# Kernel optimization log

Hardware: AMD Instinct MI355X
Metric: run time of the kernel (lower is better)

The kernel has to match this reference:

```python
import jax, jax.numpy as jnp
import numpy as np

EMBED_DIM = 1024
N, L = 4, 4096


def setup_inputs() -> dict:
    key = jax.random.key(0)
    ks = jax.random.split(key, 9)
    s = 1.0 / np.sqrt(EMBED_DIM)
    return {
        "q": jax.random.normal(ks[0], (N, L, EMBED_DIM), jnp.float32),
        "k": jax.random.normal(ks[1], (N, L, EMBED_DIM), jnp.float32),
        "v": jax.random.normal(ks[2], (N, L, EMBED_DIM), jnp.float32),
        "Wq": jax.random.normal(ks[3], (EMBED_DIM, EMBED_DIM), jnp.float32) * s,
        "bq": jax.random.normal(ks[4], (EMBED_DIM,), jnp.float32) * s,
        "Wk": jax.random.normal(ks[5], (EMBED_DIM, EMBED_DIM), jnp.float32) * s,
        "bk": jax.random.normal(ks[6], (EMBED_DIM,), jnp.float32) * s,
        "Wv": jax.random.normal(ks[7], (EMBED_DIM, EMBED_DIM), jnp.float32) * s,
        "bv": jax.random.normal(ks[8], (EMBED_DIM,), jnp.float32) * s,
    }


def reference(q, k, v, Wq, bq, Wk, bk, Wv, bv):
    scale = 1.0 / (q.shape[-1] ** 0.5)  # 1/sqrt(embed_dim), single-head
    pq = jnp.einsum("nle,fe->nlf", q, Wq) + bq  # (N, L, E)
    pk = jnp.einsum("nle,fe->nlf", k, Wk) + bk
    pv = jnp.einsum("nle,fe->nlf", v, Wv) + bv
    scores = jnp.einsum("nle,nme->nlm", pq, pk) * scale  # (N, L, L)
    attn = jax.nn.softmax(scores, axis=-1)
    return jnp.einsum("nlm,nme->nle", attn, pv)  # (N, L, E)
```

## Files before the change

### kernel.cpp

```cpp
#include <hip/hip_runtime.h>

typedef unsigned short u16;
typedef __bf16  bf16x8 __attribute__((ext_vector_type(8)));
typedef float   f32x4  __attribute__((ext_vector_type(4)));
typedef unsigned short us8 __attribute__((ext_vector_type(8)));
typedef _Float16 f16x8 __attribute__((ext_vector_type(8)));
typedef float   fl4   __attribute__((ext_vector_type(4)));

#define AS1 __attribute__((address_space(1)))
#define AS3 __attribute__((address_space(3)))

__device__ __forceinline__ u16 f2bf(float f) {
    union { float f; unsigned u; } x; x.f = f;
    unsigned r = x.u + 0x7fffu + ((x.u >> 16) & 1u);
    return (u16)(r >> 16);
}

__global__ __launch_bounds__(256) void cvt_f32_bf16(const float* __restrict__ in,
                                                    u16* __restrict__ out, int n8) {
    int i = blockIdx.x * blockDim.x + threadIdx.x;
    int stride = gridDim.x * blockDim.x;
    for (; i < n8; i += stride) {
        const fl4* p = (const fl4*)(in + (long)i * 8);
        fl4 a = p[0], b = p[1];
        us8 o;
#pragma unroll
        for (int j = 0; j < 4; ++j) { o[j] = f2bf(a[j]); o[4 + j] = f2bf(b[j]); }
        *(us8*)(out + (long)i * 8) = o;
    }
}

template <int MODE>
__global__ __launch_bounds__(512, 2) void gemm256d(const u16* __restrict__ A,
                                                   const u16* __restrict__ B,
                                                   void* __restrict__ Cout,
                                                   const float* __restrict__ bias,
                                                   float scale, int K,
                                                   int lda, int ldb, int ldc,
                                                   long sAz, long sBz, long sCz) {
    __shared__ alignas(16) char lds8[2 * 65536];

    const int t    = threadIdx.x;
    const int lane = t & 63;
    const int wid  = t >> 6;
    const int wr   = wid >> 2;
    const int wc   = wid & 3;
    const int fr   = lane & 15;
    const int kq   = lane >> 4;

    const int gx  = gridDim.x;
    const int nwg = gx * gridDim.y;
    const int wg  = blockIdx.y * gx + blockIdx.x;
    const int swz = (wg & 7) * (nwg >> 3) + (wg >> 3);
    const long brow = (long)(swz / gx) * 256;
    const long bcol = (long)(swz % gx) * 256;

    const u16* Az = A + sAz * blockIdx.z;
    const u16* Bz = B + sBz * blockIdx.z;

    const int trow = t >> 3;
    const int tc8  = ((t & 7) ^ (trow & 7)) * 8;
    long offA[4], offB[4];
#pragma unroll
    for (int r = 0; r < 4; ++r) offA[r] = (brow + r * 64 + trow) * (long)lda + tc8;
#pragma unroll
    for (int r = 0; r < 4; ++r) offB[r] = (bcol + r * 64 + trow) * (long)ldb + tc8;

    int aRow[8], bRow[4], aCh[2];
#pragma unroll
    for (int m = 0; m < 8; ++m) aRow[m] = (wr * 128 + m * 16 + fr) * 128;
#pragma unroll
    for (int n = 0; n < 4; ++n) bRow[n] = 65536 / 2 + (wc * 64 + n * 16 + fr) * 128;
#pragma unroll
    for (int ks = 0; ks < 2; ++ks) aCh[ks] = (((ks << 2) | kq) ^ (fr & 7)) * 16;

    const int NT = K >> 6;
    f32x4 acc[8][4] = {};

    {
        char* bb0 = lds8;
#pragma unroll
        for (int r = 0; r < 4; ++r)
            __builtin_amdgcn_global_load_lds((const AS1 unsigned*)(Az + offA[r]),
                                             (AS3 unsigned*)(bb0 + r * 8192 + t * 16), 16, 0, 0);
#pragma unroll
        for (int r = 0; r < 4; ++r)
            __builtin_amdgcn_global_load_lds((const AS1 unsigned*)(Bz + offB[r]),
                                             (AS3 unsigned*)(bb0 + 32768 + r * 8192 + t * 16), 16, 0, 0);
    }
    __syncthreads();

    int cur = 0;
    for (int T = 0; T < NT; ++T) {
        char* bb  = lds8 + cur * 65536;
        char* bbn = lds8 + (cur ^ 1) * 65536;

        if (T + 1 < NT) {
            const long kcol = (long)(T + 1) << 6;
#pragma unroll
            for (int r = 0; r < 4; ++r)
                __builtin_amdgcn_global_load_lds((const AS1 unsigned*)(Az + offA[r] + kcol),
                                                 (AS3 unsigned*)(bbn + r * 8192 + t * 16), 16, 0, 0);
#pragma unroll
            for (int r = 0; r < 4; ++r)
                __builtin_amdgcn_global_load_lds((const AS1 unsigned*)(Bz + offB[r] + kcol),
                                                 (AS3 unsigned*)(bbn + 32768 + r * 8192 + t * 16), 16, 0, 0);
        }

        bf16x8 bfv[2][4], afl[2][4], afh[2][4];
#pragma unroll
        for (int ks = 0; ks < 2; ++ks)
#pragma unroll
            for (int n = 0; n < 4; ++n)
                bfv[ks][n] = *(const bf16x8*)(bb + bRow[n] + aCh[ks]);
#pragma unroll
        for (int ks = 0; ks < 2; ++ks)
#pragma unroll
            for (int m = 0; m < 4; ++m)
                afl[ks][m] = *(const bf16x8*)(bb + aRow[m] + aCh[ks]);

        asm volatile("s_waitcnt lgkmcnt(0)" ::: "memory");
        __builtin_amdgcn_sched_barrier(0);
        __builtin_amdgcn_s_setprio(1);
#pragma unroll
        for (int ks = 0; ks < 2; ++ks)
#pragma unroll
            for (int m = 0; m < 4; ++m)
#pragma unroll
                for (int n = 0; n < 4; ++n)
                    acc[m][n] = __builtin_amdgcn_mfma_f32_16x16x32_bf16(afl[ks][m], bfv[ks][n], acc[m][n], 0, 0, 0);
        __builtin_amdgcn_s_setprio(0);

#pragma unroll
        for (int ks = 0; ks < 2; ++ks)
#pragma unroll
            for (int m = 0; m < 4; ++m)
                afh[ks][m] = *(const bf16x8*)(bb + aRow[4 + m] + aCh[ks]);

        asm volatile("s_waitcnt lgkmcnt(0)" ::: "memory");
        __builtin_amdgcn_sched_barrier(0);
        __builtin_amdgcn_s_setprio(1);
#pragma unroll
        for (int ks = 0; ks < 2; ++ks)
#pragma unroll
            for (int m = 0; m < 4; ++m)
#pragma unroll
                for (int n = 0; n < 4; ++n)
                    acc[4 + m][n] = __builtin_amdgcn_mfma_f32_16x16x32_bf16(afh[ks][m], bfv[ks][n], acc[4 + m][n], 0, 0, 0);
        __builtin_amdgcn_s_setprio(0);
        __builtin_amdgcn_sched_barrier(0);

        __syncthreads();
        cur ^= 1;
    }

    const long crow = brow + wr * 128;
    const long ccol = bcol + wc * 64;
    const long cz = sCz * blockIdx.z;
#pragma unroll
    for (int m = 0; m < 8; ++m) {
#pragma unroll
        for (int n = 0; n < 4; ++n) {
#pragma unroll
            for (int j = 0; j < 4; ++j) {
                long r = crow + m * 16 + kq * 4 + j;
                long c = ccol + n * 16 + fr;
                float vv = acc[m][n][j];
                if (MODE == 0)      { vv += bias[c]; ((u16*)Cout)[cz + r * ldc + c] = f2bf(vv); }
                else if (MODE == 1) { vv += bias[r]; ((u16*)Cout)[cz + r * ldc + c] = f2bf(vv); }
                else if (MODE == 2) { ((_Float16*)Cout)[cz + r * ldc + c] = (_Float16)(vv * scale); }
                else                { ((float*)Cout)[cz + r * ldc + c] = vv; }
            }
        }
    }
}

template <int MODE>
__global__ __launch_bounds__(256, 2) void gemm128(const u16* __restrict__ A,
                                                  const u16* __restrict__ B,
                                                  void* __restrict__ Cout,
                                                  const float* __restrict__ bias,
                                                  float scale, int K,
                                                  int lda, int ldb, int ldc,
                                                  long sAz, long sBz, long sCz) {
    __shared__ alignas(16) char lds8[2 * 32768];

    const int t    = threadIdx.x;
    const int lane = t & 63;
    const int wid  = t >> 6;
    const int wr   = wid >> 1;
    const int wc   = wid & 1;
    const int fr   = lane & 15;
    const int kq   = lane >> 4;

    const int gx  = gridDim.x;
    const int nwg = gx * gridDim.y;
    const int wg  = blockIdx.y * gx + blockIdx.x;
    const int swz = (wg & 7) * (nwg >> 3) + (wg >> 3);
    const long brow = (long)(swz / gx) * 128;
    const long bcol = (long)(swz % gx) * 128;

    const u16* Az = A + sAz * blockIdx.z;
    const u16* Bz = B + sBz * blockIdx.z;

    const int trow = t >> 3;
    const int tc8  = ((t & 7) ^ (trow & 7)) * 8;
    long offA[4], offB[4];
#pragma unroll
    for (int r = 0; r < 4; ++r) offA[r] = (brow + r * 32 + trow) * (long)lda + tc8;
#pragma unroll
    for (int r = 0; r < 4; ++r) offB[r] = (bcol + r * 32 + trow) * (long)ldb + tc8;

    int aRow[4], bRow[4], aCh[2];
#pragma unroll
    for (int m = 0; m < 4; ++m) aRow[m] = (wr * 64 + m * 16 + fr) * 128;
#pragma unroll
    for (int n = 0; n < 4; ++n) bRow[n] = 16384 + (wc * 64 + n * 16 + fr) * 128;
#pragma unroll
    for (int ks = 0; ks < 2; ++ks) aCh[ks] = (((ks << 2) | kq) ^ (fr & 7)) * 16;

    const int NT = K >> 6;
    f32x4 acc[4][4] = {};

    {
        char* bb0 = lds8;
#pragma unroll
        for (int r = 0; r < 4; ++r)
            __builtin_amdgcn_global_load_lds((const AS1 unsigned*)(Az + offA[r]),
                                             (AS3 unsigned*)(bb0 + r * 4096 + t * 16), 16, 0, 0);
#pragma unroll
        for (int r = 0; r < 4; ++r)
            __builtin_amdgcn_global_load_lds((const AS1 unsigned*)(Bz + offB[r]),
                                             (AS3 unsigned*)(bb0 + 16384 + r * 4096 + t * 16), 16, 0, 0);
    }
    __syncthreads();

    int cur = 0;
    for (int T = 0; T < NT; ++T) {
        char* bb  = lds8 + cur * 32768;
        char* bbn = lds8 + (cur ^ 1) * 32768;

        if (T + 1 < NT) {
            const long kcol = (long)(T + 1) << 6;
#pragma unroll
            for (int r = 0; r < 4; ++r)
                __builtin_amdgcn_global_load_lds((const AS1 unsigned*)(Az + offA[r] + kcol),
                                                 (AS3 unsigned*)(bbn + r * 4096 + t * 16), 16, 0, 0);
#pragma unroll
            for (int r = 0; r < 4; ++r)
                __builtin_amdgcn_global_load_lds((const AS1 unsigned*)(Bz + offB[r] + kcol),
                                                 (AS3 unsigned*)(bbn + 16384 + r * 4096 + t * 16), 16, 0, 0);
        }

        bf16x8 af[2][4], bfv[2][4];
#pragma unroll
        for (int ks = 0; ks < 2; ++ks)
#pragma unroll
            for (int m = 0; m < 4; ++m)
                af[ks][m] = *(const bf16x8*)(bb + aRow[m] + aCh[ks]);
#pragma unroll
        for (int ks = 0; ks < 2; ++ks)
#pragma unroll
            for (int n = 0; n < 4; ++n)
                bfv[ks][n] = *(const bf16x8*)(bb + bRow[n] + aCh[ks]);

        asm volatile("s_waitcnt lgkmcnt(0)" ::: "memory");
        __builtin_amdgcn_sched_barrier(0);
        __builtin_amdgcn_s_setprio(1);
#pragma unroll
        for (int ks = 0; ks < 2; ++ks)
#pragma unroll
            for (int m = 0; m < 4; ++m)
#pragma unroll
                for (int n = 0; n < 4; ++n)
                    acc[m][n] = __builtin_amdgcn_mfma_f32_16x16x32_bf16(af[ks][m], bfv[ks][n], acc[m][n], 0, 0, 0);
        __builtin_amdgcn_s_setprio(0);
        __builtin_amdgcn_sched_barrier(0);

        __syncthreads();
        cur ^= 1;
    }

    const long crow = brow + wr * 64;
    const long ccol = bcol + wc * 64;
    const long cz = sCz * blockIdx.z;
#pragma unroll
    for (int m = 0; m < 4; ++m) {
#pragma unroll
        for (int n = 0; n < 4; ++n) {
#pragma unroll
            for (int j = 0; j < 4; ++j) {
                long r = crow + m * 16 + kq * 4 + j;
                long c = ccol + n * 16 + fr;
                float vv = acc[m][n][j];
                if (MODE == 0)      { vv += bias[c]; ((u16*)Cout)[cz + r * ldc + c] = f2bf(vv); }
                else if (MODE == 1) { vv += bias[r]; ((u16*)Cout)[cz + r * ldc + c] = f2bf(vv); }
                else if (MODE == 2) { ((_Float16*)Cout)[cz + r * ldc + c] = (_Float16)(vv * scale); }
                else                { ((float*)Cout)[cz + r * ldc + c] = vv; }
            }
        }
    }
}

__global__ __launch_bounds__(256) void softmax_row(u16* __restrict__ S, int L) {
    const long row = blockIdx.x;
    u16* rp = S + row * L;
    const int t = threadIdx.x;
    const int lane = t & 63, wid = t >> 6;

    f16x8 h0 = *(const f16x8*)(rp + t * 16);
    f16x8 h1 = *(const f16x8*)(rp + t * 16 + 8);
    float x[16];
#pragma unroll
    for (int j = 0; j < 8; ++j) { x[j] = (float)h0[j]; x[8 + j] = (float)h1[j]; }

    float m = -1e30f;
#pragma unroll
    for (int j = 0; j < 16; ++j) m = fmaxf(m, x[j]);
#pragma unroll
    for (int o = 32; o; o >>= 1) m = fmaxf(m, __shfl_xor(m, o));

    __shared__ float redmax[4], redsum[4];
    if (lane == 0) redmax[wid] = m;
    __syncthreads();
    m = fmaxf(fmaxf(redmax[0], redmax[1]), fmaxf(redmax[2], redmax[3]));

    float e[16], s = 0.f;
#pragma unroll
    for (int j = 0; j < 16; ++j) { e[j] = __expf(x[j] - m); s += e[j]; }
#pragma unroll
    for (int o = 32; o; o >>= 1) s += __shfl_xor(s, o);
    if (lane == 0) redsum[wid] = s;
    __syncthreads();
    s = redsum[0] + redsum[1] + redsum[2] + redsum[3];
    float inv = 1.f / s;

    us8 o0, o1;
#pragma unroll
    for (int j = 0; j < 8; ++j) { o0[j] = f2bf(e[j] * inv); o1[j] = f2bf(e[8 + j] * inv); }
    *(us8*)(rp + t * 16) = o0;
    *(us8*)(rp + t * 16 + 8) = o1;
}

extern "C" void kernel_launch(void* const* d_in, const int* in_sizes, int n_in,
                              void* d_out, int out_size, void* d_ws, size_t ws_size,
                              hipStream_t stream) {
    (void)in_sizes; (void)n_in; (void)out_size; (void)ws_size;
    const float* q  = (const float*)d_in[0];
    const float* k  = (const float*)d_in[1];
    const float* v  = (const float*)d_in[2];
    const float* Wq = (const float*)d_in[3];
    const float* bq = (const float*)d_in[4];
    const float* Wk = (const float*)d_in[5];
    const float* bk = (const float*)d_in[6];
    const float* Wv = (const float*)d_in[7];
    const float* bv = (const float*)d_in[8];
    float* out = (float*)d_out;

    constexpr long MB = 1l << 20;
    char* ws = (char*)d_ws;
    u16* pq  = (u16*)(ws + 0 * MB);
    u16* pk  = (u16*)(ws + 32 * MB);
    u16* pvT = (u16*)(ws + 64 * MB);
    u16* Wqb = (u16*)(ws + 96 * MB);
    u16* Wkb = (u16*)(ws + 98 * MB);
    u16* Wvb = (u16*)(ws + 100 * MB);
    u16* qb  = (u16*)(ws + 104 * MB);
    u16* kb  = (u16*)(ws + 136 * MB);
    u16* vb  = (u16*)(ws + 168 * MB);
    u16* S2  = (u16*)(ws + 104 * MB);

    const int L = 4096, E = 1024, NB = 4;
    const int n8_x = (NB * L * E) / 8;
    const int n8_w = (E * E) / 8;

    cvt_f32_bf16<<<2048, 256, 0, stream>>>(q, qb, n8_x);
    cvt_f32_bf16<<<2048, 256, 0, stream>>>(k, kb, n8_x);
    cvt_f32_bf16<<<2048, 256, 0, stream>>>(v, vb, n8_x);
    cvt_f32_bf16<<<512, 256, 0, stream>>>(Wq, Wqb, n8_w);
    cvt_f32_bf16<<<512, 256, 0, stream>>>(Wk, Wkb, n8_w);
    cvt_f32_bf16<<<512, 256, 0, stream>>>(Wv, Wvb, n8_w);

    dim3 gproj(4, 64, 1);
    gemm256d<0><<<gproj, 512, 0, stream>>>(qb, Wqb, pq, bq, 1.f, E, E, E, E, 0, 0, 0);
    gemm256d<0><<<gproj, 512, 0, stream>>>(kb, Wkb, pk, bk, 1.f, E, E, E, E, 0, 0, 0);
    dim3 gpv(64, 4, 1);
    gemm256d<1><<<gpv, 512, 0, stream>>>(Wvb, vb, pvT, bv, 1.f, E, E, E, NB * L, 0, 0, 0);

    const float scale = 0.03125f;
    for (int p = 0; p < 2; ++p) {
        const long zb = p * 2;
        dim3 gs(16, 16, 2);
        gemm256d<2><<<gs, 512, 0, stream>>>(pq + zb * L * E, pk + zb * L * E, (void*)S2,
                                            nullptr, scale, E, E, E, L,
                                            (long)L * E, (long)L * E, (long)L * L);
        softmax_row<<<2 * L, 256, 0, stream>>>(S2, L);
        dim3 gp(8, 32, 2);
        gemm128<3><<<gp, 256, 0, stream>>>(S2, pvT + zb * L, out + zb * L * E,
                                           nullptr, 1.f, L, L, NB * L, E,
                                           (long)L * L, (long)L, (long)L * E);
    }
}
```

Before: 475.6 us.

## Batch conversions, process all four batches at once, and drop explicit LDS waits

Merges the six fp32-to-bf16 conversion launches into two multi-input launches. When the workspace is large enough, computes the scores, softmax and PV product for all four batches in one pass instead of two, and switches the PV GEMM to the 256-tile kernel. Removes the explicit lgkmcnt waits and sched barriers before the MFMA blocks so the compiler can interleave LDS reads with math. This cuts launch count and adds parallelism per launch, but needs a larger workspace and depends on the compiler inserting correct waits.

```diff
diff --git a/kernel.cpp b/kernel.cpp
--- a/kernel.cpp
+++ b/kernel.cpp
@@ -16,8 +16,14 @@
     return (u16)(r >> 16);
 }
 
-__global__ __launch_bounds__(256) void cvt_f32_bf16(const float* __restrict__ in,
-                                                    u16* __restrict__ out, int n8) {
+__global__ __launch_bounds__(256) void cvt3_f32_bf16(const float* __restrict__ in0,
+                                                     const float* __restrict__ in1,
+                                                     const float* __restrict__ in2,
+                                                     u16* __restrict__ out0,
+                                                     u16* __restrict__ out1,
+                                                     u16* __restrict__ out2, int n8) {
+    const float* in = blockIdx.y == 0 ? in0 : (blockIdx.y == 1 ? in1 : in2);
+    u16* out        = blockIdx.y == 0 ? out0 : (blockIdx.y == 1 ? out1 : out2);
     int i = blockIdx.x * blockDim.x + threadIdx.x;
     int stride = gridDim.x * blockDim.x;
     for (; i < n8; i += stride) {
@@ -70,7 +76,7 @@
 #pragma unroll
     for (int m = 0; m < 8; ++m) aRow[m] = (wr * 128 + m * 16 + fr) * 128;
 #pragma unroll
-    for (int n = 0; n < 4; ++n) bRow[n] = 65536 / 2 + (wc * 64 + n * 16 + fr) * 128;
+    for (int n = 0; n < 4; ++n) bRow[n] = 32768 + (wc * 64 + n * 16 + fr) * 128;
 #pragma unroll
     for (int ks = 0; ks < 2; ++ks) aCh[ks] = (((ks << 2) | kq) ^ (fr & 7)) * 16;
 
@@ -119,8 +125,6 @@
             for (int m = 0; m < 4; ++m)
                 afl[ks][m] = *(const bf16x8*)(bb + aRow[m] + aCh[ks]);
 
-        asm volatile("s_waitcnt lgkmcnt(0)" ::: "memory");
-        __builtin_amdgcn_sched_barrier(0);
         __builtin_amdgcn_s_setprio(1);
 #pragma unroll
         for (int ks = 0; ks < 2; ++ks)
@@ -137,8 +141,6 @@
             for (int m = 0; m < 4; ++m)
                 afh[ks][m] = *(const bf16x8*)(bb + aRow[4 + m] + aCh[ks]);
 
-        asm volatile("s_waitcnt lgkmcnt(0)" ::: "memory");
-        __builtin_amdgcn_sched_barrier(0);
         __builtin_amdgcn_s_setprio(1);
 #pragma unroll
         for (int ks = 0; ks < 2; ++ks)
@@ -148,7 +150,6 @@
                 for (int n = 0; n < 4; ++n)
                     acc[4 + m][n] = __builtin_amdgcn_mfma_f32_16x16x32_bf16(afh[ks][m], bfv[ks][n], acc[4 + m][n], 0, 0, 0);
         __builtin_amdgcn_s_setprio(0);
-        __builtin_amdgcn_sched_barrier(0);
 
         __syncthreads();
         cur ^= 1;
@@ -264,8 +265,6 @@
             for (int n = 0; n < 4; ++n)
                 bfv[ks][n] = *(const bf16x8*)(bb + bRow[n] + aCh[ks]);
 
-        asm volatile("s_waitcnt lgkmcnt(0)" ::: "memory");
-        __builtin_amdgcn_sched_barrier(0);
         __builtin_amdgcn_s_setprio(1);
 #pragma unroll
         for (int ks = 0; ks < 2; ++ks)
@@ -275,7 +274,6 @@
                 for (int n = 0; n < 4; ++n)
                     acc[m][n] = __builtin_amdgcn_mfma_f32_16x16x32_bf16(af[ks][m], bfv[ks][n], acc[m][n], 0, 0, 0);
         __builtin_amdgcn_s_setprio(0);
-        __builtin_amdgcn_sched_barrier(0);
 
         __syncthreads();
         cur ^= 1;
@@ -345,7 +343,7 @@
 extern "C" void kernel_launch(void* const* d_in, const int* in_sizes, int n_in,
                               void* d_out, int out_size, void* d_ws, size_t ws_size,
                               hipStream_t stream) {
-    (void)in_sizes; (void)n_in; (void)out_size; (void)ws_size;
+    (void)in_sizes; (void)n_in; (void)out_size;
     const float* q  = (const float*)d_in[0];
     const float* k  = (const float*)d_in[1];
     const float* v  = (const float*)d_in[2];
@@ -368,18 +366,15 @@
     u16* qb  = (u16*)(ws + 104 * MB);
     u16* kb  = (u16*)(ws + 136 * MB);
     u16* vb  = (u16*)(ws + 168 * MB);
-    u16* S2  = (u16*)(ws + 104 * MB);
+    u16* S4  = (u16*)(ws + 104 * MB);
 
     const int L = 4096, E = 1024, NB = 4;
     const int n8_x = (NB * L * E) / 8;
     const int n8_w = (E * E) / 8;
-
-    cvt_f32_bf16<<<2048, 256, 0, stream>>>(q, qb, n8_x);
-    cvt_f32_bf16<<<2048, 256, 0, stream>>>(k, kb, n8_x);
-    cvt_f32_bf16<<<2048, 256, 0, stream>>>(v, vb, n8_x);
-    cvt_f32_bf16<<<512, 256, 0, stream>>>(Wq, Wqb, n8_w);
-    cvt_f32_bf16<<<512, 256, 0, stream>>>(Wk, Wkb, n8_w);
-    cvt_f32_bf16<<<512, 256, 0, stream>>>(Wv, Wvb, n8_w);
+    const bool z4 = ws_size >= (size_t)233 * MB;
+
+    cvt3_f32_bf16<<<dim3(1024, 3), 256, 0, stream>>>(q, k, v, qb, kb, vb, n8_x);
+    cvt3_f32_bf16<<<dim3(256, 3), 256, 0, stream>>>(Wq, Wk, Wv, Wqb, Wkb, Wvb, n8_w);
 
     dim3 gproj(4, 64, 1);
     gemm256d<0><<<gproj, 512, 0, stream>>>(qb, Wqb, pq, bq, 1.f, E, E, E, E, 0, 0, 0);
@@ -388,16 +383,25 @@
     gemm256d<1><<<gpv, 512, 0, stream>>>(Wvb, vb, pvT, bv, 1.f, E, E, E, NB * L, 0, 0, 0);
 
     const float scale = 0.03125f;
-    for (int p = 0; p < 2; ++p) {
-        const long zb = p * 2;
-        dim3 gs(16, 16, 2);
-        gemm256d<2><<<gs, 512, 0, stream>>>(pq + zb * L * E, pk + zb * L * E, (void*)S2,
-                                            nullptr, scale, E, E, E, L,
-                                            (long)L * E, (long)L * E, (long)L * L);
-        softmax_row<<<2 * L, 256, 0, stream>>>(S2, L);
-        dim3 gp(8, 32, 2);
-        gemm128<3><<<gp, 256, 0, stream>>>(S2, pvT + zb * L, out + zb * L * E,
-                                           nullptr, 1.f, L, L, NB * L, E,
-                                           (long)L * L, (long)L, (long)L * E);
-    }
-}
+    if (z4) {
+        gemm256d<2><<<dim3(16, 16, 4), 512, 0, stream>>>(pq, pk, (void*)S4,
+                                                         nullptr, scale, E, E, E, L,
+                                                         (long)L * E, (long)L * E, (long)L * L);
+        softmax_row<<<NB * L, 256, 0, stream>>>(S4, L);
+        gemm256d<3><<<dim3(4, 16, 4), 512, 0, stream>>>(S4, pvT, out,
+                                                        nullptr, 1.f, L, L, NB * L, E,
+                                                        (long)L * L, (long)L, (long)L * E);
+    } else {
+        u16* S2 = S4;
+        for (int p = 0; p < 2; ++p) {
+            const long zb = p * 2;
+            gemm256d<2><<<dim3(16, 16, 2), 512, 0, stream>>>(pq + zb * L * E, pk + zb * L * E, (void*)S2,
+                                                             nullptr, scale, E, E, E, L,
+                                                             (long)L * E, (long)L * E, (long)L * L);
+            softmax_row<<<2 * L, 256, 0, stream>>>(S2, L);
+            gemm128<3><<<dim3(8, 32, 2), 256, 0, stream>>>(S2, pvT + zb * L, out + zb * L * E,
+                                                           nullptr, 1.f, L, L, NB * L, E,
+                                                           (long)L * L, (long)L, (long)L * E);
+        }
+    }
+}
```

Result: faster. 451.0 us (-5.2%).
